# Performance work log

Measured on AMD Instinct MI355X. Metric: run time of the kernel, lower is better.

The kernel has to match this reference:

```python
import jax, jax.numpy as jnp
import numpy as np

IMG_FEAT = 2048
HIDDEN = 1024
K_TIMES = 3
GLIMPSE = 8
BA_HIDDEN = K_TIMES * HIDDEN  # 3072


def setup_inputs() -> dict:
    key = jax.random.key(0)
    ks = jax.random.split(key, 9)
    b, n_v, n_q = 64, 128, 32
    v = jax.random.normal(ks[0], (b, n_v, IMG_FEAT), dtype=jnp.float32)
    q = jax.random.normal(ks[1], (b, n_q, HIDDEN), dtype=jnp.float32)
    # weight-normed Linear params (weight_norm with dim=None -> scalar g)
    v_w = jax.random.normal(ks[2], (BA_HIDDEN, IMG_FEAT), dtype=jnp.float32) * 0.02
    v_g = jnp.asarray(jnp.linalg.norm(v_w), dtype=jnp.float32)
    v_b = jnp.zeros((BA_HIDDEN,), dtype=jnp.float32)
    q_w = jax.random.normal(ks[3], (BA_HIDDEN, HIDDEN), dtype=jnp.float32) * 0.02
    q_g = jnp.asarray(jnp.linalg.norm(q_w), dtype=jnp.float32)
    q_b = jnp.zeros((BA_HIDDEN,), dtype=jnp.float32)
    h_mat = jax.random.normal(ks[4], (1, GLIMPSE, 1, BA_HIDDEN), dtype=jnp.float32)
    h_bias = jax.random.normal(ks[5], (1, GLIMPSE, 1, 1), dtype=jnp.float32)
    return {"v": v, "q": q, "v_w": v_w, "v_g": v_g, "v_b": v_b,
            "q_w": q_w, "q_g": q_g, "q_b": q_b,
            "h_mat": h_mat, "h_bias": h_bias}


def _wn_linear_relu(x, w, g, b):
    # weight_norm(dim=None): w_eff = g * w / ||w||_F (scalar g)
    w_eff = (g / jnp.linalg.norm(w)) * w
    return jax.nn.relu(jnp.einsum('bnd,kd->bnk', x, w_eff) + b)


def reference(v, q, v_w, v_g, v_b, q_w, q_g, q_b, h_mat, h_bias):
    # dropout layers are identity in eval mode
    v_ = _wn_linear_relu(v, v_w, v_g, v_b)  # [b, n_v, K]
    q_ = _wn_linear_relu(q, q_w, q_g, q_b)  # [b, n_q, K]
    # einsum('xhyk,bvk,bqk->bhvq') with h_mat [1,g,1,K]
    hm = h_mat[0, :, 0, :]  # [g, K]
    logits = jnp.einsum('hk,bvk,bqk->bhvq', hm, v_, q_) + h_bias
    return logits
```

## Files before the change

kernel.cpp:

```cpp
#include <hip/hip_runtime.h>

typedef __attribute__((ext_vector_type(8))) __bf16 bf16x8;
typedef __attribute__((ext_vector_type(4))) float f32x4;
typedef const __attribute__((address_space(1))) unsigned int gas_u32;
typedef __attribute__((address_space(3))) unsigned int las_u32;

__device__ __forceinline__ unsigned short f2bf(float f) {
  unsigned u = __builtin_bit_cast(unsigned, f);
  u = (u + 0x7FFFu + ((u >> 16) & 1u)) >> 16;
  return (unsigned short)u;
}
__device__ __forceinline__ float bf2f(unsigned short h) {
  return __builtin_bit_cast(float, (unsigned)h << 16);
}

__global__ __launch_bounds__(256) void k_sumsq(const float* __restrict__ w, int n4,
                                               float* __restrict__ out) {
  int tid = threadIdx.x;
  float s = 0.f;
  for (int i = blockIdx.x * 256 + tid; i < n4; i += gridDim.x * 256) {
    float4 v = ((const float4*)w)[i];
    s += v.x * v.x + v.y * v.y + v.z * v.z + v.w * v.w;
  }
  for (int off = 32; off; off >>= 1) s += __shfl_down(s, off);
  __shared__ float red[4];
  if ((tid & 63) == 0) red[tid >> 6] = s;
  __syncthreads();
  if (tid == 0) atomicAdd(out, red[0] + red[1] + red[2] + red[3]);
}

__global__ __launch_bounds__(256) void k_cvt(const float* __restrict__ in,
                                             unsigned short* __restrict__ out, int n8) {
  for (int i = blockIdx.x * 256 + threadIdx.x; i < n8; i += gridDim.x * 256) {
    float4 a = ((const float4*)in)[2 * i];
    float4 b = ((const float4*)in)[2 * i + 1];
    uint4 o;
    o.x = f2bf(a.x) | ((unsigned)f2bf(a.y) << 16);
    o.y = f2bf(a.z) | ((unsigned)f2bf(a.w) << 16);
    o.z = f2bf(b.x) | ((unsigned)f2bf(b.y) << 16);
    o.w = f2bf(b.z) | ((unsigned)f2bf(b.w) << 16);
    ((uint4*)out)[i] = o;
  }
}

__global__ __launch_bounds__(512, 2) void k_gemm_wn(
    const unsigned short* __restrict__ A, const unsigned short* __restrict__ B,
    const float* __restrict__ bias, const float* __restrict__ gptr,
    const float* __restrict__ ssptr, unsigned short* __restrict__ C,
    int M, int N, int K, int nbn) {
  __shared__ __align__(16) unsigned short lA[2 * 128 * 64];
  __shared__ __align__(16) unsigned short lB[2 * 384 * 64];
  const int tid = threadIdx.x;
  const int wid = tid >> 6, lane = tid & 63;
  const int l15 = lane & 15, l4 = lane >> 4;
  const int wm = wid >> 2, wn = wid & 3;
  const int rr = tid >> 3;
  const int scol = ((tid & 7) ^ (rr & 7)) << 3;

  int nwg = gridDim.x;
  int wg = (blockIdx.x & 7) * (nwg >> 3) + (blockIdx.x >> 3);
  int bm = wg / nbn, bn = wg % nbn;

  const unsigned short* Ab = A + (size_t)bm * 128 * K;
  const unsigned short* Bb = B + (size_t)bn * 384 * K;
  const int nt = K >> 6;

#define STAGEU(U, TS)                                                            \
  {                                                                              \
    int ts_ = (TS) < nt ? (TS) : nt - 1;                                         \
    if ((U) < 2) {                                                               \
      __builtin_amdgcn_global_load_lds(                                          \
          (gas_u32*)(Ab + (size_t)((U)*64 + rr) * K + ts_ * 64 + scol),          \
          (las_u32*)(lA + ((TS)&1) * 8192 + (U)*4096 + tid * 8), 16, 0, 0);      \
    } else {                                                                     \
      __builtin_amdgcn_global_load_lds(                                          \
          (gas_u32*)(Bb + (size_t)(((U)-2) * 64 + rr) * K + ts_ * 64 + scol),    \
          (las_u32*)(lB + ((TS)&1) * 24576 + ((U)-2) * 4096 + tid * 8), 16, 0,   \
          0);                                                                    \
    }                                                                            \
  }

#define LDSA(DST, MQ, TP)                                                        \
  _Pragma("unroll") for (int i2 = 0; i2 < 2; ++i2) {                             \
    int rl = wm * 64 + ((MQ)*2 + i2) * 16 + l15;                                 \
    const unsigned short* ap = lA + (TP)*8192 + rl * 64;                         \
    int s8 = rl & 7;                                                             \
    DST[i2][0] = *(const bf16x8*)(ap + ((l4 ^ s8) << 3));                        \
    DST[i2][1] = *(const bf16x8*)(ap + (((4 | l4) ^ s8) << 3));                  \
  }

#define LDSB(DST, NQ, TP)                                                        \
  _Pragma("unroll") for (int j3 = 0; j3 < 3; ++j3) {                             \
    int rl = wn * 96 + ((NQ)*3 + j3) * 16 + l15;                                 \
    const unsigned short* bp = lB + (TP)*24576 + rl * 64;                        \
    int s8 = rl & 7;                                                             \
    DST[j3][0] = *(const bf16x8*)(bp + ((l4 ^ s8) << 3));                        \
    DST[j3][1] = *(const bf16x8*)(bp + (((4 | l4) ^ s8) << 3));                  \
  }

#define MFMA12(MQ, NQ, AF, BF)                                                   \
  _Pragma("unroll") for (int ks = 0; ks < 2; ++ks)                               \
  _Pragma("unroll") for (int i2 = 0; i2 < 2; ++i2)                               \
  _Pragma("unroll") for (int j3 = 0; j3 < 3; ++j3)                               \
    acc[(MQ)*2 + i2][(NQ)*3 + j3] = __builtin_amdgcn_mfma_f32_16x16x32_bf16(     \
        AF[i2][ks], BF[j3][ks], acc[(MQ)*2 + i2][(NQ)*3 + j3], 0, 0, 0);

  f32x4 acc[4][6] = {};
  bf16x8 a0_[2][2], a1_[2][2], b0_[3][2], b1_[3][2];

  STAGEU(0, 0) STAGEU(1, 0) STAGEU(2, 0) STAGEU(3, 0)
  STAGEU(4, 0) STAGEU(5, 0) STAGEU(6, 0) STAGEU(7, 0)
  STAGEU(0, 1) STAGEU(1, 1)
  asm volatile("s_waitcnt vmcnt(2)" ::: "memory");
  __builtin_amdgcn_sched_barrier(0);
  __builtin_amdgcn_s_barrier();
  LDSA(a0_, 0, 0)
  STAGEU(2, 1) STAGEU(3, 1)
  LDSB(b0_, 0, 0)

  for (int t = 0; t < nt; ++t) {
    const int cp = t & 1, np = (t + 1) & 1;
    LDSB(b1_, 1, cp)
    STAGEU(4, t + 1) STAGEU(5, t + 1)
    __builtin_amdgcn_s_setprio(1);
    MFMA12(0, 0, a0_, b0_)
    __builtin_amdgcn_s_setprio(0);
    LDSA(a1_, 1, cp)
    STAGEU(6, t + 1) STAGEU(7, t + 1)
    __builtin_amdgcn_s_setprio(1);
    MFMA12(0, 1, a0_, b1_)
    __builtin_amdgcn_s_setprio(0);
    asm volatile("s_waitcnt lgkmcnt(0)" ::: "memory");
    asm volatile("s_waitcnt vmcnt(6)" ::: "memory");
    __builtin_amdgcn_sched_barrier(0);
    __builtin_amdgcn_s_barrier();
    LDSA(a0_, 0, np)
    STAGEU(0, t + 2) STAGEU(1, t + 2)
    __builtin_amdgcn_s_setprio(1);
    MFMA12(1, 0, a1_, b0_)
    __builtin_amdgcn_s_setprio(0);
    asm volatile("s_waitcnt vmcnt(2)" ::: "memory");
    __builtin_amdgcn_sched_barrier(0);
    __builtin_amdgcn_s_barrier();
    LDSB(b0_, 0, np)
    STAGEU(2, t + 2) STAGEU(3, t + 2)
    __builtin_amdgcn_s_setprio(1);
    MFMA12(1, 1, a1_, b1_)
    __builtin_amdgcn_s_setprio(0);
  }

  asm volatile("s_waitcnt vmcnt(0)" ::: "memory");

  float s = gptr[0] / sqrtf(ssptr[0]);
#pragma unroll
  for (int nj = 0; nj < 6; ++nj) {
    int gcol = bn * 384 + wn * 96 + nj * 16 + l15;
    float bv = bias[gcol];
#pragma unroll
    for (int mi = 0; mi < 4; ++mi) {
#pragma unroll
      for (int r = 0; r < 4; ++r) {
        int grow = bm * 128 + wm * 64 + mi * 16 + l4 * 4 + r;
        float v = fmaxf(acc[mi][nj][r] * s + bv, 0.f);
        C[(size_t)grow * N + gcol] = f2bf(v);
      }
    }
  }
#undef STAGEU
#undef LDSA
#undef LDSB
#undef MFMA12
}

__global__ __launch_bounds__(256, 2) void k_gemm_bt(
    const unsigned short* __restrict__ A, const unsigned short* __restrict__ B,
    const float* __restrict__ bias, const float* __restrict__ gptr,
    const float* __restrict__ ssptr, unsigned short* __restrict__ C,
    int M, int N, int K, int nbn) {
  __shared__ __align__(16) unsigned short lA[128 * 64];
  __shared__ __align__(16) unsigned short lB[128 * 64];
  int tid = threadIdx.x;
  int wid = tid >> 6, lane = tid & 63;
  int l15 = lane & 15, l4 = lane >> 4;
  int w0 = wid >> 1, w1 = wid & 1;

  int nwg = gridDim.x;
  int wg = blockIdx.x;
  int cpx = nwg >> 3;
  wg = (wg & 7) * cpx + (wg >> 3);
  int bm = wg / nbn, bn = wg % nbn;

  const unsigned short* Ab = A + (size_t)bm * 128 * K;
  const unsigned short* Bb = B + (size_t)bn * 128 * K;

  f32x4 acc[4][4] = {};

  for (int k0 = 0; k0 < K; k0 += 64) {
    __syncthreads();
#pragma unroll
    for (int i = 0; i < 4; ++i) {
      int ebase = (i * 4 + wid) << 9;
      int eoff = ebase + lane * 8;
      int row = eoff >> 6, col = eoff & 63;
      __builtin_amdgcn_global_load_lds(
          (gas_u32*)(Ab + (size_t)row * K + k0 + col),
          (las_u32*)(lA + ebase), 16, 0, 0);
      __builtin_amdgcn_global_load_lds(
          (gas_u32*)(Bb + (size_t)row * K + k0 + col),
          (las_u32*)(lB + ebase), 16, 0, 0);
    }
    __syncthreads();
#pragma unroll
    for (int ks = 0; ks < 2; ++ks) {
      bf16x8 af[4], bfr[4];
#pragma unroll
      for (int mi = 0; mi < 4; ++mi)
        af[mi] = *(const bf16x8*)(lA + ((w0 * 64 + mi * 16 + l15) * 64 + ks * 32 + l4 * 8));
#pragma unroll
      for (int nj = 0; nj < 4; ++nj)
        bfr[nj] = *(const bf16x8*)(lB + ((w1 * 64 + nj * 16 + l15) * 64 + ks * 32 + l4 * 8));
#pragma unroll
      for (int mi = 0; mi < 4; ++mi)
#pragma unroll
        for (int nj = 0; nj < 4; ++nj)
          acc[mi][nj] =
              __builtin_amdgcn_mfma_f32_16x16x32_bf16(af[mi], bfr[nj], acc[mi][nj], 0, 0, 0);
    }
  }

  float s = gptr[0] / sqrtf(ssptr[0]);
#pragma unroll
  for (int mi = 0; mi < 4; ++mi)
#pragma unroll
    for (int nj = 0; nj < 4; ++nj) {
      int col = bn * 128 + w1 * 64 + nj * 16 + l15;
      float bv = bias[col];
#pragma unroll
      for (int r = 0; r < 4; ++r) {
        int row = bm * 128 + w0 * 64 + mi * 16 + l4 * 4 + r;
        float v = fmaxf(acc[mi][nj][r] * s + bv, 0.f);
        C[(size_t)row * N + col] = f2bf(v);
      }
    }
}

__global__ __launch_bounds__(256, 2) void k_glimpse2(
    const unsigned short* __restrict__ Vh, const unsigned short* __restrict__ Qh,
    const float* __restrict__ hmat, const float* __restrict__ hbias,
    float* __restrict__ out) {
  __shared__ __align__(16) unsigned short lV[128 * 64];
  __shared__ __align__(16) unsigned short lQ[2][32 * 64];
  int tid = threadIdx.x;
  int wid = tid >> 6, lane = tid & 63;
  int l15 = lane & 15, l4 = lane >> 4;

  int id = blockIdx.x;
  int b = id & 63, h2 = id >> 6;

  const unsigned short* Vb = Vh + (size_t)b * 128 * 3072;
  const unsigned short* Qb = Qh + (size_t)b * 32 * 3072;
  const float* hr0 = hmat + h2 * 3072;
  const float* hr1 = hmat + (h2 + 4) * 3072;

  f32x4 acc[2][2][2] = {};

  int eoff = tid * 8;
  int qr = eoff >> 6, qc = eoff & 63;

  for (int k0 = 0; k0 < 3072; k0 += 64) {
    __syncthreads();
#pragma unroll
    for (int i = 0; i < 4; ++i) {
      int ebase = (i * 4 + wid) << 9;
      int eo = ebase + lane * 8;
      int row = eo >> 6, col = eo & 63;
      __builtin_amdgcn_global_load_lds(
          (gas_u32*)(Vb + (size_t)row * 3072 + k0 + col),
          (las_u32*)(lV + ebase), 16, 0, 0);
    }
    {
      uint4 qv = *(const uint4*)(Qb + (size_t)qr * 3072 + k0 + qc);
      float e0 = bf2f((unsigned short)(qv.x & 0xffff)), e1 = bf2f((unsigned short)(qv.x >> 16));
      float e2 = bf2f((unsigned short)(qv.y & 0xffff)), e3 = bf2f((unsigned short)(qv.y >> 16));
      float e4 = bf2f((unsigned short)(qv.z & 0xffff)), e5 = bf2f((unsigned short)(qv.z >> 16));
      float e6 = bf2f((unsigned short)(qv.w & 0xffff)), e7 = bf2f((unsigned short)(qv.w >> 16));
      const float* hp0 = hr0 + k0 + qc;
      const float* hp1 = hr1 + k0 + qc;
      float4 p00 = ((const float4*)hp0)[0], p01 = ((const float4*)hp0)[1];
      float4 p10 = ((const float4*)hp1)[0], p11 = ((const float4*)hp1)[1];
      uint4 o0, o1;
      o0.x = f2bf(e0 * p00.x) | ((unsigned)f2bf(e1 * p00.y) << 16);
      o0.y = f2bf(e2 * p00.z) | ((unsigned)f2bf(e3 * p00.w) << 16);
      o0.z = f2bf(e4 * p01.x) | ((unsigned)f2bf(e5 * p01.y) << 16);
      o0.w = f2bf(e6 * p01.z) | ((unsigned)f2bf(e7 * p01.w) << 16);
      o1.x = f2bf(e0 * p10.x) | ((unsigned)f2bf(e1 * p10.y) << 16);
      o1.y = f2bf(e2 * p10.z) | ((unsigned)f2bf(e3 * p10.w) << 16);
      o1.z = f2bf(e4 * p11.x) | ((unsigned)f2bf(e5 * p11.y) << 16);
      o1.w = f2bf(e6 * p11.z) | ((unsigned)f2bf(e7 * p11.w) << 16);
      *(uint4*)(lQ[0] + eoff) = o0;
      *(uint4*)(lQ[1] + eoff) = o1;
    }
    __syncthreads();
#pragma unroll
    for (int ks = 0; ks < 2; ++ks) {
      bf16x8 af[2];
#pragma unroll
      for (int mi = 0; mi < 2; ++mi)
        af[mi] = *(const bf16x8*)(lV + ((wid * 32 + mi * 16 + l15) * 64 + ks * 32 + l4 * 8));
#pragma unroll
      for (int hh = 0; hh < 2; ++hh) {
        bf16x8 bf2[2];
#pragma unroll
        for (int nj = 0; nj < 2; ++nj)
          bf2[nj] = *(const bf16x8*)(lQ[hh] + ((nj * 16 + l15) * 64 + ks * 32 + l4 * 8));
#pragma unroll
        for (int mi = 0; mi < 2; ++mi)
#pragma unroll
          for (int nj = 0; nj < 2; ++nj)
            acc[hh][mi][nj] = __builtin_amdgcn_mfma_f32_16x16x32_bf16(
                af[mi], bf2[nj], acc[hh][mi][nj], 0, 0, 0);
      }
    }
  }

#pragma unroll
  for (int hh = 0; hh < 2; ++hh) {
    int h = h2 + hh * 4;
    float hb = hbias[h];
    float* ob = out + (size_t)(b * 8 + h) * 128 * 32;
#pragma unroll
    for (int mi = 0; mi < 2; ++mi)
#pragma unroll
      for (int nj = 0; nj < 2; ++nj)
#pragma unroll
        for (int r = 0; r < 4; ++r) {
          int row = wid * 32 + mi * 16 + l4 * 4 + r;
          int col = nj * 16 + l15;
          ob[row * 32 + col] = acc[hh][mi][nj][r] + hb;
        }
  }
}

extern "C" void kernel_launch(void* const* d_in, const int* in_sizes, int n_in,
                              void* d_out, int out_size, void* d_ws, size_t ws_size,
                              hipStream_t stream) {
  const float* v = (const float*)d_in[0];
  const float* q = (const float*)d_in[1];
  const float* v_w = (const float*)d_in[2];
  const float* v_g = (const float*)d_in[3];
  const float* v_b = (const float*)d_in[4];
  const float* q_w = (const float*)d_in[5];
  const float* q_g = (const float*)d_in[6];
  const float* q_b = (const float*)d_in[7];
  const float* hmat = (const float*)d_in[8];
  const float* hbias = (const float*)d_in[9];
  float* out = (float*)d_out;

  const size_t n_v = 16777216;
  const size_t n_vw = 6291456;
  const size_t n_q = 2097152;
  const size_t n_qw = 3145728;
  const size_t n_vh = 25165824;
  const size_t n_qh = 6291456;

  char* ws = (char*)d_ws;
  float* ss = (float*)ws;
  size_t off = 256;
  unsigned short* v_bf = (unsigned short*)(ws + off);  off += n_v * 2;
  unsigned short* vw_bf = (unsigned short*)(ws + off); off += n_vw * 2;
  unsigned short* q_bf = (unsigned short*)(ws + off);  off += n_q * 2;
  unsigned short* qw_bf = (unsigned short*)(ws + off); off += n_qw * 2;
  unsigned short* v_h = (unsigned short*)(ws + off);   off += n_vh * 2;
  unsigned short* q_h = (unsigned short*)(ws + off);   off += n_qh * 2;

  (void)hipMemsetAsync(ss, 0, 8, stream);
  k_sumsq<<<512, 256, 0, stream>>>(v_w, (int)(n_vw / 4), ss + 0);
  k_sumsq<<<512, 256, 0, stream>>>(q_w, (int)(n_qw / 4), ss + 1);

  k_cvt<<<1024, 256, 0, stream>>>(v, v_bf, (int)(n_v / 8));
  k_cvt<<<1024, 256, 0, stream>>>(v_w, vw_bf, (int)(n_vw / 8));
  k_cvt<<<1024, 256, 0, stream>>>(q, q_bf, (int)(n_q / 8));
  k_cvt<<<1024, 256, 0, stream>>>(q_w, qw_bf, (int)(n_qw / 8));

  k_gemm_wn<<<512, 512, 0, stream>>>(v_bf, vw_bf, v_b, v_g, ss + 0, v_h,
                                     8192, 3072, 2048, 8);
  k_gemm_bt<<<384, 256, 0, stream>>>(q_bf, qw_bf, q_b, q_g, ss + 1, q_h,
                                     2048, 3072, 1024, 24);

  k_glimpse2<<<256, 256, 0, stream>>>(v_h, q_h, hmat, hbias, out);
}
```

Before: 237.6 us.

## Fuse weight sumsq into conversion, remap GEMM tiles, pipeline glimpse kernel

Merges the Frobenius-norm reduction into the bf16 conversion of the weights, so each weight matrix is read once instead of twice and two launches disappear. Both GEMMs switch from row-major to column-major tile indexing (bm = wg % nbm), which changes how L2 reuse of the weight tiles works. The big GEMM moves some B-tile prefetches to a different point in the loop. The glimpse kernel becomes a triple-buffered V pipeline with double-buffered Q, using register prefetch and explicit waitcnt, so loads overlap the MFMAs at the cost of more LDS.

```diff
diff --git a/kernel.cpp b/kernel.cpp
--- a/kernel.cpp
+++ b/kernel.cpp
@@ -12,21 +12,6 @@
 }
 __device__ __forceinline__ float bf2f(unsigned short h) {
   return __builtin_bit_cast(float, (unsigned)h << 16);
-}
-
-__global__ __launch_bounds__(256) void k_sumsq(const float* __restrict__ w, int n4,
-                                               float* __restrict__ out) {
-  int tid = threadIdx.x;
-  float s = 0.f;
-  for (int i = blockIdx.x * 256 + tid; i < n4; i += gridDim.x * 256) {
-    float4 v = ((const float4*)w)[i];
-    s += v.x * v.x + v.y * v.y + v.z * v.z + v.w * v.w;
-  }
-  for (int off = 32; off; off >>= 1) s += __shfl_down(s, off);
-  __shared__ float red[4];
-  if ((tid & 63) == 0) red[tid >> 6] = s;
-  __syncthreads();
-  if (tid == 0) atomicAdd(out, red[0] + red[1] + red[2] + red[3]);
 }
 
 __global__ __launch_bounds__(256) void k_cvt(const float* __restrict__ in,
@@ -43,11 +28,35 @@
   }
 }
 
+__global__ __launch_bounds__(256) void k_cvt_sq(const float* __restrict__ in,
+                                                unsigned short* __restrict__ out, int n8,
+                                                float* __restrict__ ssout) {
+  int tid = threadIdx.x;
+  float s = 0.f;
+  for (int i = blockIdx.x * 256 + tid; i < n8; i += gridDim.x * 256) {
+    float4 a = ((const float4*)in)[2 * i];
+    float4 b = ((const float4*)in)[2 * i + 1];
+    s += a.x * a.x + a.y * a.y + a.z * a.z + a.w * a.w;
+    s += b.x * b.x + b.y * b.y + b.z * b.z + b.w * b.w;
+    uint4 o;
+    o.x = f2bf(a.x) | ((unsigned)f2bf(a.y) << 16);
+    o.y = f2bf(a.z) | ((unsigned)f2bf(a.w) << 16);
+    o.z = f2bf(b.x) | ((unsigned)f2bf(b.y) << 16);
+    o.w = f2bf(b.z) | ((unsigned)f2bf(b.w) << 16);
+    ((uint4*)out)[i] = o;
+  }
+  for (int off = 32; off; off >>= 1) s += __shfl_down(s, off);
+  __shared__ float red[4];
+  if ((tid & 63) == 0) red[tid >> 6] = s;
+  __syncthreads();
+  if (tid == 0) atomicAdd(ssout, red[0] + red[1] + red[2] + red[3]);
+}
+
 __global__ __launch_bounds__(512, 2) void k_gemm_wn(
     const unsigned short* __restrict__ A, const unsigned short* __restrict__ B,
     const float* __restrict__ bias, const float* __restrict__ gptr,
     const float* __restrict__ ssptr, unsigned short* __restrict__ C,
-    int M, int N, int K, int nbn) {
+    int M, int N, int K, int nbm) {
   __shared__ __align__(16) unsigned short lA[2 * 128 * 64];
   __shared__ __align__(16) unsigned short lB[2 * 384 * 64];
   const int tid = threadIdx.x;
@@ -59,7 +68,7 @@
 
   int nwg = gridDim.x;
   int wg = (blockIdx.x & 7) * (nwg >> 3) + (blockIdx.x >> 3);
-  int bm = wg / nbn, bn = wg % nbn;
+  int bm = wg % nbm, bn = wg / nbm;
 
   const unsigned short* Ab = A + (size_t)bm * 128 * K;
   const unsigned short* Bb = B + (size_t)bn * 384 * K;
@@ -115,7 +124,7 @@
   __builtin_amdgcn_sched_barrier(0);
   __builtin_amdgcn_s_barrier();
   LDSA(a0_, 0, 0)
-  STAGEU(2, 1) STAGEU(3, 1)
+  STAGEU(2, 1) STAGEU(3, 1) STAGEU(6, 1) STAGEU(7, 1)
   LDSB(b0_, 0, 0)
 
   for (int t = 0; t < nt; ++t) {
@@ -126,7 +135,6 @@
     MFMA12(0, 0, a0_, b0_)
     __builtin_amdgcn_s_setprio(0);
     LDSA(a1_, 1, cp)
-    STAGEU(6, t + 1) STAGEU(7, t + 1)
     __builtin_amdgcn_s_setprio(1);
     MFMA12(0, 1, a0_, b1_)
     __builtin_amdgcn_s_setprio(0);
@@ -143,7 +151,7 @@
     __builtin_amdgcn_sched_barrier(0);
     __builtin_amdgcn_s_barrier();
     LDSB(b0_, 0, np)
-    STAGEU(2, t + 2) STAGEU(3, t + 2)
+    STAGEU(2, t + 2) STAGEU(3, t + 2) STAGEU(6, t + 2) STAGEU(7, t + 2)
     __builtin_amdgcn_s_setprio(1);
     MFMA12(1, 1, a1_, b1_)
     __builtin_amdgcn_s_setprio(0);
@@ -176,7 +184,7 @@
     const unsigned short* __restrict__ A, const unsigned short* __restrict__ B,
     const float* __restrict__ bias, const float* __restrict__ gptr,
     const float* __restrict__ ssptr, unsigned short* __restrict__ C,
-    int M, int N, int K, int nbn) {
+    int M, int N, int K, int nbm) {
   __shared__ __align__(16) unsigned short lA[128 * 64];
   __shared__ __align__(16) unsigned short lB[128 * 64];
   int tid = threadIdx.x;
@@ -185,10 +193,8 @@
   int w0 = wid >> 1, w1 = wid & 1;
 
   int nwg = gridDim.x;
-  int wg = blockIdx.x;
-  int cpx = nwg >> 3;
-  wg = (wg & 7) * cpx + (wg >> 3);
-  int bm = wg / nbn, bn = wg % nbn;
+  int wg = (blockIdx.x & 7) * (nwg >> 3) + (blockIdx.x >> 3);
+  int bm = wg % nbm, bn = wg / nbm;
 
   const unsigned short* Ab = A + (size_t)bm * 128 * K;
   const unsigned short* Bb = B + (size_t)bn * 128 * K;
@@ -244,12 +250,12 @@
     }
 }
 
-__global__ __launch_bounds__(256, 2) void k_glimpse2(
+__global__ __launch_bounds__(256, 2) void k_glimpse3(
     const unsigned short* __restrict__ Vh, const unsigned short* __restrict__ Qh,
     const float* __restrict__ hmat, const float* __restrict__ hbias,
     float* __restrict__ out) {
-  __shared__ __align__(16) unsigned short lV[128 * 64];
-  __shared__ __align__(16) unsigned short lQ[2][32 * 64];
+  __shared__ __align__(16) unsigned short lV[3][128 * 64];
+  __shared__ __align__(16) unsigned short lQ[2][2][32 * 64];
   int tid = threadIdx.x;
   int wid = tid >> 6, lane = tid & 63;
   int l15 = lane & 15, l4 = lane >> 4;
@@ -263,65 +269,104 @@
   const float* hr1 = hmat + (h2 + 4) * 3072;
 
   f32x4 acc[2][2][2] = {};
-
   int eoff = tid * 8;
   int qr = eoff >> 6, qc = eoff & 63;
-
-  for (int k0 = 0; k0 < 3072; k0 += 64) {
-    __syncthreads();
-#pragma unroll
-    for (int i = 0; i < 4; ++i) {
-      int ebase = (i * 4 + wid) << 9;
-      int eo = ebase + lane * 8;
-      int row = eo >> 6, col = eo & 63;
-      __builtin_amdgcn_global_load_lds(
-          (gas_u32*)(Vb + (size_t)row * 3072 + k0 + col),
-          (las_u32*)(lV + ebase), 16, 0, 0);
-    }
-    {
-      uint4 qv = *(const uint4*)(Qb + (size_t)qr * 3072 + k0 + qc);
-      float e0 = bf2f((unsigned short)(qv.x & 0xffff)), e1 = bf2f((unsigned short)(qv.x >> 16));
-      float e2 = bf2f((unsigned short)(qv.y & 0xffff)), e3 = bf2f((unsigned short)(qv.y >> 16));
-      float e4 = bf2f((unsigned short)(qv.z & 0xffff)), e5 = bf2f((unsigned short)(qv.z >> 16));
-      float e6 = bf2f((unsigned short)(qv.w & 0xffff)), e7 = bf2f((unsigned short)(qv.w >> 16));
-      const float* hp0 = hr0 + k0 + qc;
-      const float* hp1 = hr1 + k0 + qc;
-      float4 p00 = ((const float4*)hp0)[0], p01 = ((const float4*)hp0)[1];
-      float4 p10 = ((const float4*)hp1)[0], p11 = ((const float4*)hp1)[1];
-      uint4 o0, o1;
-      o0.x = f2bf(e0 * p00.x) | ((unsigned)f2bf(e1 * p00.y) << 16);
-      o0.y = f2bf(e2 * p00.z) | ((unsigned)f2bf(e3 * p00.w) << 16);
-      o0.z = f2bf(e4 * p01.x) | ((unsigned)f2bf(e5 * p01.y) << 16);
-      o0.w = f2bf(e6 * p01.z) | ((unsigned)f2bf(e7 * p01.w) << 16);
-      o1.x = f2bf(e0 * p10.x) | ((unsigned)f2bf(e1 * p10.y) << 16);
-      o1.y = f2bf(e2 * p10.z) | ((unsigned)f2bf(e3 * p10.w) << 16);
-      o1.z = f2bf(e4 * p11.x) | ((unsigned)f2bf(e5 * p11.y) << 16);
-      o1.w = f2bf(e6 * p11.z) | ((unsigned)f2bf(e7 * p11.w) << 16);
-      *(uint4*)(lQ[0] + eoff) = o0;
-      *(uint4*)(lQ[1] + eoff) = o1;
-    }
-    __syncthreads();
-#pragma unroll
-    for (int ks = 0; ks < 2; ++ks) {
-      bf16x8 af[2];
-#pragma unroll
-      for (int mi = 0; mi < 2; ++mi)
-        af[mi] = *(const bf16x8*)(lV + ((wid * 32 + mi * 16 + l15) * 64 + ks * 32 + l4 * 8));
-#pragma unroll
-      for (int hh = 0; hh < 2; ++hh) {
-        bf16x8 bf2[2];
-#pragma unroll
-        for (int nj = 0; nj < 2; ++nj)
-          bf2[nj] = *(const bf16x8*)(lQ[hh] + ((nj * 16 + l15) * 64 + ks * 32 + l4 * 8));
-#pragma unroll
-        for (int mi = 0; mi < 2; ++mi)
-#pragma unroll
-          for (int nj = 0; nj < 2; ++nj)
-            acc[hh][mi][nj] = __builtin_amdgcn_mfma_f32_16x16x32_bf16(
-                af[mi], bf2[nj], acc[hh][mi][nj], 0, 0, 0);
-      }
-    }
-  }
+  const int NT = 48;
+
+#define VSTAGE(T, SLOT)                                                          \
+  {                                                                              \
+    int tc = (T) < NT ? (T) : NT - 1;                                            \
+    _Pragma("unroll") for (int i = 0; i < 4; ++i) {                              \
+      int ebase = (i * 4 + wid) << 9;                                            \
+      int eo = ebase + lane * 8;                                                 \
+      int row = eo >> 6, col = eo & 63;                                          \
+      __builtin_amdgcn_global_load_lds(                                          \
+          (gas_u32*)(Vb + (size_t)row * 3072 + tc * 64 + col),                   \
+          (las_u32*)(&lV[SLOT][0] + ebase), 16, 0, 0);                           \
+    }                                                                            \
+  }
+
+#define QLOAD(T, RQ, H0A, H0B, H1A, H1B)                                         \
+  {                                                                              \
+    int tc = (T) < NT ? (T) : NT - 1;                                            \
+    RQ = *(const uint4*)(Qb + (size_t)qr * 3072 + tc * 64 + qc);                 \
+    const float* hp0 = hr0 + tc * 64 + qc;                                       \
+    const float* hp1 = hr1 + tc * 64 + qc;                                       \
+    H0A = ((const float4*)hp0)[0];                                               \
+    H0B = ((const float4*)hp0)[1];                                               \
+    H1A = ((const float4*)hp1)[0];                                               \
+    H1B = ((const float4*)hp1)[1];                                               \
+  }
+
+#define QWRITE(CB, RQ, H0A, H0B, H1A, H1B)                                       \
+  {                                                                              \
+    float e0 = bf2f((unsigned short)(RQ.x & 0xffff));                            \
+    float e1 = bf2f((unsigned short)(RQ.x >> 16));                               \
+    float e2 = bf2f((unsigned short)(RQ.y & 0xffff));                            \
+    float e3 = bf2f((unsigned short)(RQ.y >> 16));                               \
+    float e4 = bf2f((unsigned short)(RQ.z & 0xffff));                            \
+    float e5 = bf2f((unsigned short)(RQ.z >> 16));                               \
+    float e6 = bf2f((unsigned short)(RQ.w & 0xffff));                            \
+    float e7 = bf2f((unsigned short)(RQ.w >> 16));                               \
+    uint4 o0, o1;                                                                \
+    o0.x = f2bf(e0 * H0A.x) | ((unsigned)f2bf(e1 * H0A.y) << 16);                \
+    o0.y = f2bf(e2 * H0A.z) | ((unsigned)f2bf(e3 * H0A.w) << 16);                \
+    o0.z = f2bf(e4 * H0B.x) | ((unsigned)f2bf(e5 * H0B.y) << 16);                \
+    o0.w = f2bf(e6 * H0B.z) | ((unsigned)f2bf(e7 * H0B.w) << 16);                \
+    o1.x = f2bf(e0 * H1A.x) | ((unsigned)f2bf(e1 * H1A.y) << 16);                \
+    o1.y = f2bf(e2 * H1A.z) | ((unsigned)f2bf(e3 * H1A.w) << 16);                \
+    o1.z = f2bf(e4 * H1B.x) | ((unsigned)f2bf(e5 * H1B.y) << 16);                \
+    o1.w = f2bf(e6 * H1B.z) | ((unsigned)f2bf(e7 * H1B.w) << 16);                \
+    *(uint4*)(&lQ[CB][0][0] + eoff) = o0;                                        \
+    *(uint4*)(&lQ[CB][1][0] + eoff) = o1;                                        \
+  }
+
+#define GMFMA(SLOT, CB)                                                          \
+  _Pragma("unroll") for (int ks = 0; ks < 2; ++ks) {                             \
+    bf16x8 af[2];                                                                \
+    _Pragma("unroll") for (int mi = 0; mi < 2; ++mi)                             \
+      af[mi] = *(const bf16x8*)(&lV[SLOT][0] +                                   \
+                                ((wid * 32 + mi * 16 + l15) * 64 + ks * 32 + l4 * 8)); \
+    _Pragma("unroll") for (int hh = 0; hh < 2; ++hh) {                           \
+      bf16x8 bq[2];                                                              \
+      _Pragma("unroll") for (int nj = 0; nj < 2; ++nj)                           \
+        bq[nj] = *(const bf16x8*)(&lQ[CB][hh][0] +                               \
+                                  ((nj * 16 + l15) * 64 + ks * 32 + l4 * 8));    \
+      _Pragma("unroll") for (int mi = 0; mi < 2; ++mi)                           \
+        _Pragma("unroll") for (int nj = 0; nj < 2; ++nj)                         \
+          acc[hh][mi][nj] = __builtin_amdgcn_mfma_f32_16x16x32_bf16(             \
+              af[mi], bq[nj], acc[hh][mi][nj], 0, 0, 0);                         \
+    }                                                                            \
+  }
+
+#define GBODY(T, CQ, CH0A, CH0B, CH1A, CH1B, NQ, NH0A, NH0B, NH1A, NH1B)         \
+  {                                                                              \
+    QLOAD((T) + 2, NQ, NH0A, NH0B, NH1A, NH1B)                                   \
+    asm volatile("s_waitcnt vmcnt(9)" ::: "memory");                             \
+    asm volatile("s_waitcnt lgkmcnt(0)" ::: "memory");                           \
+    __builtin_amdgcn_sched_barrier(0);                                           \
+    __builtin_amdgcn_s_barrier();                                                \
+    VSTAGE((T) + 2, ((T) + 2) % 3)                                               \
+    QWRITE(((T) + 1) & 1, CQ, CH0A, CH0B, CH1A, CH1B)                            \
+    GMFMA((T) % 3, (T) & 1)                                                      \
+  }
+
+  uint4 aq, bq_;
+  float4 ah0a, ah0b, ah1a, ah1b, bh0a, bh0b, bh1a, bh1b;
+
+  QLOAD(0, aq, ah0a, ah0b, ah1a, ah1b)
+  QLOAD(1, bq_, bh0a, bh0b, bh1a, bh1b)
+  VSTAGE(0, 0)
+  VSTAGE(1, 1)
+  asm volatile("s_waitcnt vmcnt(13)" ::: "memory");
+  __builtin_amdgcn_sched_barrier(0);
+  QWRITE(0, aq, ah0a, ah0b, ah1a, ah1b)
+
+  for (int t = 0; t < NT; t += 2) {
+    GBODY(t, bq_, bh0a, bh0b, bh1a, bh1b, aq, ah0a, ah0b, ah1a, ah1b)
+    GBODY(t + 1, aq, ah0a, ah0b, ah1a, ah1b, bq_, bh0a, bh0b, bh1a, bh1b)
+  }
+  asm volatile("s_waitcnt vmcnt(0) lgkmcnt(0)" ::: "memory");
 
 #pragma unroll
   for (int hh = 0; hh < 2; ++hh) {
@@ -339,6 +384,11 @@
           ob[row * 32 + col] = acc[hh][mi][nj][r] + hb;
         }
   }
+#undef VSTAGE
+#undef QLOAD
+#undef QWRITE
+#undef GMFMA
+#undef GBODY
 }
 
 extern "C" void kernel_launch(void* const* d_in, const int* in_sizes, int n_in,
@@ -374,18 +424,15 @@
   unsigned short* q_h = (unsigned short*)(ws + off);   off += n_qh * 2;
 
   (void)hipMemsetAsync(ss, 0, 8, stream);
-  k_sumsq<<<512, 256, 0, stream>>>(v_w, (int)(n_vw / 4), ss + 0);
-  k_sumsq<<<512, 256, 0, stream>>>(q_w, (int)(n_qw / 4), ss + 1);
-
+  k_cvt_sq<<<512, 256, 0, stream>>>(v_w, vw_bf, (int)(n_vw / 8), ss + 0);
+  k_cvt_sq<<<512, 256, 0, stream>>>(q_w, qw_bf, (int)(n_qw / 8), ss + 1);
   k_cvt<<<1024, 256, 0, stream>>>(v, v_bf, (int)(n_v / 8));
-  k_cvt<<<1024, 256, 0, stream>>>(v_w, vw_bf, (int)(n_vw / 8));
   k_cvt<<<1024, 256, 0, stream>>>(q, q_bf, (int)(n_q / 8));
-  k_cvt<<<1024, 256, 0, stream>>>(q_w, qw_bf, (int)(n_qw / 8));
 
   k_gemm_wn<<<512, 512, 0, stream>>>(v_bf, vw_bf, v_b, v_g, ss + 0, v_h,
-                                     8192, 3072, 2048, 8);
+                                     8192, 3072, 2048, 64);
   k_gemm_bt<<<384, 256, 0, stream>>>(q_bf, qw_bf, q_b, q_g, ss + 1, q_h,
-                                     2048, 3072, 1024, 24);
-
-  k_glimpse2<<<256, 256, 0, stream>>>(v_h, q_h, hmat, hbias, out);
-}
+                                     2048, 3072, 1024, 16);
+
+  k_glimpse3<<<256, 256, 0, stream>>>(v_h, q_h, hmat, hbias, out);
+}
```

After: 236.4 us. No clear change (-0.5%).
